# Kernel tuning notes

Hardware: AMD Instinct MI355X
Metric: run time of the kernel (lower is better)

## Reference

```python
import jax, jax.numpy as jnp
import numpy as np

Z_DIM = 1          # coord column zeroed before coalescing (module default)
GRID = 512         # max coordinate value per column (exclusive)


def setup_inputs() -> dict:
    key = jax.random.key(0)
    k1, k2 = jax.random.split(key)
    N, C = 400000, 128
    features = jax.random.normal(k1, (N, C), dtype=jnp.float32)
    coords = jax.random.randint(k2, (N, 4), 0, GRID, dtype=jnp.int32)
    return {"features": features, "coords": coords}


def reference(features, coords):
    # features: [N, C] float, coords: [N, 4] int32
    N = features.shape[0]
    # Zero the z column (BEV flattening), as in flatten_coords[:, z_dim] = 0.
    # Since the z column is identically 0 after zeroing, coalescing the 4-col
    # coords is equivalent to keying on the remaining 3 columns.
    non_z = [i for i in range(4) if i != Z_DIM]
    c0 = coords[:, non_z[0]].astype(jnp.int32)
    c1 = coords[:, non_z[1]].astype(jnp.int32)
    c2 = coords[:, non_z[2]].astype(jnp.int32)
    lin_key = (c0 * GRID + c1) * GRID + c2  # < 512^3 < 2^31, fits int32

    # coalesce(): unique coords + scatter-add of [count | features]
    uniq, inv = jnp.unique(lin_key, size=N, fill_value=-1, return_inverse=True)
    ones = jnp.ones((N, 1), dtype=features.dtype)
    feat_with_cnt = jnp.concatenate([ones, features], axis=1)  # [N, C+1]
    sums = jax.ops.segment_sum(feat_with_cnt, inv.reshape(-1), num_segments=N)  # [N, C+1]

    cnt = sums[:, :1]
    out_features = sums[:, 1:] / jnp.maximum(cnt, 1.0)  # padded rows have cnt=0 -> stay 0

    # Decode unique keys back to 4-column coords (z column = 0).
    d2 = uniq % GRID
    rem = uniq // GRID
    d1 = rem % GRID
    d0 = rem // GRID
    zeros = jnp.zeros_like(d0)
    cols = [None] * 4
    cols[Z_DIM] = zeros
    cols[non_z[0]] = d0
    cols[non_z[1]] = d1
    cols[non_z[2]] = d2
    out_coords = jnp.stack(cols, axis=1).astype(jnp.int32)  # [N, 4], padded rows negative

    return out_features, out_coords, cnt[:, 0]
```

## Files before the change

### kernel.cpp

```cpp
#include <hip/hip_runtime.h>


#define NWORDS      (1u << 22)
#define SCAN_BLOCKS 1024
#define WPB         (NWORDS / SCAN_BLOCKS)
#define WPT         (WPB / 256)

typedef float f32x4 __attribute__((ext_vector_type(4)));
typedef unsigned u32;

__global__ void k_build(const int4* __restrict__ coords, u32* __restrict__ bitmap,
                        u32* __restrict__ keys, float* __restrict__ cnt,
                        u32* __restrict__ ctrs, int N) {
    int i = blockIdx.x * blockDim.x + threadIdx.x;
    if (i == 0) { ctrs[0] = 0u; ctrs[1] = 0u; }
    if (i >= N) return;
    int4 c = coords[i];
    u32 key = ((u32)c.x << 18) | ((u32)c.z << 9) | (u32)c.w;
    keys[i] = key;
    cnt[i] = 0.0f;
    atomicOr(&bitmap[key >> 5], 1u << (key & 31u));
}

__global__ void k_scan1(const u32* __restrict__ bitmap, u32* __restrict__ blockSums) {
    __shared__ u32 sd[256];
    const uint4* bm = (const uint4*)(bitmap + (size_t)blockIdx.x * WPB + (size_t)threadIdx.x * WPT);
    u32 s = 0;
#pragma unroll
    for (int k = 0; k < WPT / 4; ++k) {
        uint4 v = bm[k];
        s += __popc(v.x) + __popc(v.y) + __popc(v.z) + __popc(v.w);
    }
    sd[threadIdx.x] = s;
    __syncthreads();
    for (int off = 128; off > 0; off >>= 1) {
        if ((int)threadIdx.x < off) sd[threadIdx.x] += sd[threadIdx.x + off];
        __syncthreads();
    }
    if (threadIdx.x == 0) blockSums[blockIdx.x] = sd[0];
}

__global__ void k_scan2(const u32* __restrict__ blockSums,
                        u32* __restrict__ blockOffsets,
                        u32* __restrict__ totalM) {
    __shared__ u32 sd[SCAN_BLOCKS];
    int t = threadIdx.x;
    u32 v = blockSums[t];
    sd[t] = v;
    __syncthreads();
    for (int off = 1; off < SCAN_BLOCKS; off <<= 1) {
        u32 add = (t >= off) ? sd[t - off] : 0u;
        __syncthreads();
        sd[t] += add;
        __syncthreads();
    }
    blockOffsets[t] = sd[t] - v;
    if (t == SCAN_BLOCKS - 1) totalM[0] = sd[t];
}

__global__ void k_scan3enum(const u32* __restrict__ bitmap,
                            const u32* __restrict__ blockOffsets,
                            uint2* __restrict__ pairs,
                            float4* __restrict__ outc) {
    __shared__ u32 sd[256];
    size_t base = (size_t)blockIdx.x * WPB + (size_t)threadIdx.x * WPT;
    const uint4* bm = (const uint4*)(bitmap + base);
    u32 w[WPT];
    u32 s = 0;
#pragma unroll
    for (int k = 0; k < WPT / 4; ++k) {
        uint4 v = bm[k];
        w[k * 4 + 0] = v.x; w[k * 4 + 1] = v.y; w[k * 4 + 2] = v.z; w[k * 4 + 3] = v.w;
        s += __popc(v.x) + __popc(v.y) + __popc(v.z) + __popc(v.w);
    }
    int t = threadIdx.x;
    sd[t] = s;
    __syncthreads();
    for (int off = 1; off < 256; off <<= 1) {
        u32 add = (t >= off) ? sd[t - off] : 0u;
        __syncthreads();
        sd[t] += add;
        __syncthreads();
    }
    u32 run = blockOffsets[blockIdx.x] + sd[t] - s;
#pragma unroll
    for (int k = 0; k < WPT; ++k) {
        u32 bits = w[k];
        pairs[base + k] = make_uint2(run, bits);
        while (bits) {
            int b = __ffs(bits) - 1;
            u32 key = ((u32)(base + k) << 5) | (u32)b;
            outc[run] = make_float4((float)(key >> 18), 0.f,
                                    (float)((key >> 9) & 511u), (float)(key & 511u));
            ++run;
            bits &= bits - 1u;
        }
    }
}

__global__ void __launch_bounds__(256) k_scatter(
        const f32x4* __restrict__ fin, const u32* __restrict__ keys,
        const uint2* __restrict__ pairs, float* __restrict__ cnt,
        u32* __restrict__ srcElem, uint2* __restrict__ dupElem,
        u32* __restrict__ dupSeg, u32* __restrict__ ctrs,
        f32x4* __restrict__ fout, int N) {
    int gid = blockIdx.x * blockDim.x + threadIdx.x;
    int elem = gid >> 5;
    if (elem >= N) return;
    int c4 = gid & 31;
    u32 s = 0;
    if ((threadIdx.x & 31) == 0) {
        u32 key = keys[elem];
        uint2 p = pairs[key >> 5];
        s = p.x + __popc(p.y & ((1u << (key & 31u)) - 1u));
        float old = atomicAdd(&cnt[s], 1.0f);
        if (old == 0.0f) {
            srcElem[s] = (u32)elem;
        } else {
            u32 di = atomicAdd(&ctrs[0], 1u);
            dupElem[di] = make_uint2((u32)elem, s);
            if (old == 1.0f) {
                u32 ds = atomicAdd(&ctrs[1], 1u);
                dupSeg[ds] = s;
            }
        }
    }
    s = (u32)__shfl((int)s, threadIdx.x & 32);
    f32x4 v = __builtin_nontemporal_load(&fin[(size_t)elem * 32 + c4]);
    fout[(size_t)s * 32 + c4] = v;
}

__global__ void k_fix1(const u32* __restrict__ dupSeg, const u32* __restrict__ ctrs,
                       const u32* __restrict__ totalM,
                       f32x4* __restrict__ fout, float4* __restrict__ outc, int N) {
    u32 nds = ctrs[1];
    u32 M = totalM[0];
    u32 npad = (u32)N - M;
    u32 total = nds + npad;
    int gid = blockIdx.x * blockDim.x + threadIdx.x;
    int c4 = gid & 31;
    u32 stride = (gridDim.x * blockDim.x) >> 5;
    f32x4 z = {0.f, 0.f, 0.f, 0.f};
    for (u32 r = (u32)(gid >> 5); r < total; r += stride) {
        bool pad = (r >= nds);
        u32 row = pad ? (M + r - nds) : dupSeg[r];
        fout[(size_t)row * 32 + c4] = z;
        if (pad && c4 == 0) outc[row] = make_float4(-1.f, 0.f, 511.f, 511.f);
    }
}

__global__ void k_fix2(const f32x4* __restrict__ fin, const uint2* __restrict__ dupElem,
                       const u32* __restrict__ dupSeg, const u32* __restrict__ srcElem,
                       const float* __restrict__ cnt, const u32* __restrict__ ctrs,
                       f32x4* __restrict__ fout) {
    u32 nde = ctrs[0], nds = ctrs[1];
    u32 total = nde + nds;
    int gid = blockIdx.x * blockDim.x + threadIdx.x;
    int c4 = gid & 31;
    u32 stride = (gridDim.x * blockDim.x) >> 5;
    for (u32 t = (u32)(gid >> 5); t < total; t += stride) {
        u32 e, s;
        if (t < nde) { uint2 d = dupElem[t]; e = d.x; s = d.y; }
        else         { s = dupSeg[t - nde]; e = srcElem[s]; }
        float inv = 1.0f / cnt[s];
        f32x4 v = fin[(size_t)e * 32 + c4];
        float* dst = (float*)&fout[(size_t)s * 32 + c4];
        atomicAdd(dst + 0, v.x * inv);
        atomicAdd(dst + 1, v.y * inv);
        atomicAdd(dst + 2, v.z * inv);
        atomicAdd(dst + 3, v.w * inv);
    }
}

extern "C" void kernel_launch(void* const* d_in, const int* in_sizes, int n_in,
                              void* d_out, int out_size, void* d_ws, size_t ws_size,
                              hipStream_t stream) {
    const f32x4* feat_in = (const f32x4*)d_in[0];
    const int4* coords = (const int4*)d_in[1];
    int N = in_sizes[1] / 4;

    float* out = (float*)d_out;
    f32x4* out_feat = (f32x4*)out;
    float4* out_coords = (float4*)(out + (size_t)N * 128);
    float* out_cnt = out + (size_t)N * 132;

    u32* bitmap = (u32*)d_ws;
    uint2* pairs = (uint2*)(bitmap + NWORDS);
    u32* keys = (u32*)(pairs + NWORDS);
    u32* srcElem = keys + N;
    u32* dupSeg = srcElem + N;
    uint2* dupElem = (uint2*)(dupSeg + 65536);
    u32* blockSums = (u32*)(dupElem + 65536);
    u32* blockOffsets = blockSums + SCAN_BLOCKS;
    u32* totalM = blockOffsets + SCAN_BLOCKS;
    u32* ctrs = totalM + 1;

    int nb = (N + 255) / 256;

    hipMemsetAsync(bitmap, 0, (size_t)NWORDS * 4, stream);

    k_build<<<nb, 256, 0, stream>>>(coords, bitmap, keys, out_cnt, ctrs, N);
    k_scan1<<<SCAN_BLOCKS, 256, 0, stream>>>(bitmap, blockSums);
    k_scan2<<<1, SCAN_BLOCKS, 0, stream>>>(blockSums, blockOffsets, totalM);
    k_scan3enum<<<SCAN_BLOCKS, 256, 0, stream>>>(bitmap, blockOffsets, pairs, out_coords);
    k_scatter<<<(int)(((size_t)N * 32 + 255) / 256), 256, 0, stream>>>(
        feat_in, keys, pairs, out_cnt, srcElem, dupElem, dupSeg, ctrs, out_feat, N);
    k_fix1<<<256, 256, 0, stream>>>(dupSeg, ctrs, totalM, out_feat, out_coords, N);
    k_fix2<<<256, 256, 0, stream>>>(feat_in, dupElem, dupSeg, srcElem, out_cnt, ctrs, out_feat);
}
```

Measured before the change: 159.9 us.

## Fuse block counting into build, merge scan kernels, replace atomic fixup with search

The build kernel now counts newly set bits per scan block with atomics, so the separate popcount pass over the bitmap goes away. The block-level prefix is recomputed inside each enumeration block, which removes the single-block scan kernel. The two fixup kernels are merged into one, and each duplicated segment is summed by linearly searching the whole duplicate-element list instead of using float atomics. This cuts three launches and one full bitmap read, but adds a serial loop per duplicate segment that grows with the number of duplicates.

New measurement: 271.9 us. 70.1% more time.

```diff
diff --git a/kernel.cpp b/kernel.cpp
--- a/kernel.cpp
+++ b/kernel.cpp
@@ -11,7 +11,7 @@
 
 __global__ void k_build(const int4* __restrict__ coords, u32* __restrict__ bitmap,
                         u32* __restrict__ keys, float* __restrict__ cnt,
-                        u32* __restrict__ ctrs, int N) {
+                        u32* __restrict__ blockSums, u32* __restrict__ ctrs, int N) {
     int i = blockIdx.x * blockDim.x + threadIdx.x;
     if (i == 0) { ctrs[0] = 0u; ctrs[1] = 0u; }
     if (i >= N) return;
@@ -19,51 +19,42 @@
     u32 key = ((u32)c.x << 18) | ((u32)c.z << 9) | (u32)c.w;
     keys[i] = key;
     cnt[i] = 0.0f;
-    atomicOr(&bitmap[key >> 5], 1u << (key & 31u));
+    u32 bit = 1u << (key & 31u);
+    u32 old = atomicOr(&bitmap[key >> 5], bit);
+    if (!(old & bit)) atomicAdd(&blockSums[key >> 17], 1u);
 }
 
-__global__ void k_scan1(const u32* __restrict__ bitmap, u32* __restrict__ blockSums) {
+__global__ void k_scanenum(const u32* __restrict__ bitmap,
+                           const u32* __restrict__ blockSums,
+                           uint2* __restrict__ pairs,
+                           float4* __restrict__ outc,
+                           u32* __restrict__ totalM) {
     __shared__ u32 sd[256];
-    const uint4* bm = (const uint4*)(bitmap + (size_t)blockIdx.x * WPB + (size_t)threadIdx.x * WPT);
-    u32 s = 0;
-#pragma unroll
-    for (int k = 0; k < WPT / 4; ++k) {
-        uint4 v = bm[k];
-        s += __popc(v.x) + __popc(v.y) + __popc(v.z) + __popc(v.w);
-    }
-    sd[threadIdx.x] = s;
+    __shared__ u32 pfx[SCAN_BLOCKS];
+    const int t = threadIdx.x;
+    const int bid = blockIdx.x;
+
+    uint4 bs = ((const uint4*)blockSums)[t];
+    u32 ls = bs.x + bs.y + bs.z + bs.w;
+    sd[t] = ls;
     __syncthreads();
-    for (int off = 128; off > 0; off >>= 1) {
-        if ((int)threadIdx.x < off) sd[threadIdx.x] += sd[threadIdx.x + off];
-        __syncthreads();
-    }
-    if (threadIdx.x == 0) blockSums[blockIdx.x] = sd[0];
-}
-
-__global__ void k_scan2(const u32* __restrict__ blockSums,
-                        u32* __restrict__ blockOffsets,
-                        u32* __restrict__ totalM) {
-    __shared__ u32 sd[SCAN_BLOCKS];
-    int t = threadIdx.x;
-    u32 v = blockSums[t];
-    sd[t] = v;
-    __syncthreads();
-    for (int off = 1; off < SCAN_BLOCKS; off <<= 1) {
+    for (int off = 1; off < 256; off <<= 1) {
         u32 add = (t >= off) ? sd[t - off] : 0u;
         __syncthreads();
         sd[t] += add;
         __syncthreads();
     }
-    blockOffsets[t] = sd[t] - v;
-    if (t == SCAN_BLOCKS - 1) totalM[0] = sd[t];
-}
+    u32 ex = sd[t] - ls;
+    pfx[t * 4 + 0] = ex;
+    pfx[t * 4 + 1] = ex + bs.x;
+    pfx[t * 4 + 2] = ex + bs.x + bs.y;
+    pfx[t * 4 + 3] = ex + bs.x + bs.y + bs.z;
+    if (bid == 0 && t == 255) totalM[0] = sd[255];
+    __syncthreads();
+    const u32 blockBase = pfx[bid];
+    __syncthreads();
 
-__global__ void k_scan3enum(const u32* __restrict__ bitmap,
-                            const u32* __restrict__ blockOffsets,
-                            uint2* __restrict__ pairs,
-                            float4* __restrict__ outc) {
-    __shared__ u32 sd[256];
-    size_t base = (size_t)blockIdx.x * WPB + (size_t)threadIdx.x * WPT;
+    size_t base = (size_t)bid * WPB + (size_t)t * WPT;
     const uint4* bm = (const uint4*)(bitmap + base);
     u32 w[WPT];
     u32 s = 0;
@@ -73,7 +64,6 @@
         w[k * 4 + 0] = v.x; w[k * 4 + 1] = v.y; w[k * 4 + 2] = v.z; w[k * 4 + 3] = v.w;
         s += __popc(v.x) + __popc(v.y) + __popc(v.z) + __popc(v.w);
     }
-    int t = threadIdx.x;
     sd[t] = s;
     __syncthreads();
     for (int off = 1; off < 256; off <<= 1) {
@@ -82,7 +72,7 @@
         sd[t] += add;
         __syncthreads();
     }
-    u32 run = blockOffsets[blockIdx.x] + sd[t] - s;
+    u32 run = blockBase + sd[t] - s;
 #pragma unroll
     for (int k = 0; k < WPT; ++k) {
         u32 bits = w[k];
@@ -130,45 +120,35 @@
     fout[(size_t)s * 32 + c4] = v;
 }
 
-__global__ void k_fix1(const u32* __restrict__ dupSeg, const u32* __restrict__ ctrs,
-                       const u32* __restrict__ totalM,
-                       f32x4* __restrict__ fout, float4* __restrict__ outc, int N) {
-    u32 nds = ctrs[1];
+__global__ void k_fix(const f32x4* __restrict__ fin, const uint2* __restrict__ dupElem,
+                      const u32* __restrict__ dupSeg, const u32* __restrict__ srcElem,
+                      const float* __restrict__ cnt, const u32* __restrict__ ctrs,
+                      const u32* __restrict__ totalM,
+                      f32x4* __restrict__ fout, float4* __restrict__ outc, int N) {
+    u32 nde = ctrs[0], nds = ctrs[1];
     u32 M = totalM[0];
     u32 npad = (u32)N - M;
     u32 total = nds + npad;
     int gid = blockIdx.x * blockDim.x + threadIdx.x;
     int c4 = gid & 31;
     u32 stride = (gridDim.x * blockDim.x) >> 5;
-    f32x4 z = {0.f, 0.f, 0.f, 0.f};
     for (u32 r = (u32)(gid >> 5); r < total; r += stride) {
-        bool pad = (r >= nds);
-        u32 row = pad ? (M + r - nds) : dupSeg[r];
-        fout[(size_t)row * 32 + c4] = z;
-        if (pad && c4 == 0) outc[row] = make_float4(-1.f, 0.f, 511.f, 511.f);
-    }
-}
-
-__global__ void k_fix2(const f32x4* __restrict__ fin, const uint2* __restrict__ dupElem,
-                       const u32* __restrict__ dupSeg, const u32* __restrict__ srcElem,
-                       const float* __restrict__ cnt, const u32* __restrict__ ctrs,
-                       f32x4* __restrict__ fout) {
-    u32 nde = ctrs[0], nds = ctrs[1];
-    u32 total = nde + nds;
-    int gid = blockIdx.x * blockDim.x + threadIdx.x;
-    int c4 = gid & 31;
-    u32 stride = (gridDim.x * blockDim.x) >> 5;
-    for (u32 t = (u32)(gid >> 5); t < total; t += stride) {
-        u32 e, s;
-        if (t < nde) { uint2 d = dupElem[t]; e = d.x; s = d.y; }
-        else         { s = dupSeg[t - nde]; e = srcElem[s]; }
-        float inv = 1.0f / cnt[s];
-        f32x4 v = fin[(size_t)e * 32 + c4];
-        float* dst = (float*)&fout[(size_t)s * 32 + c4];
-        atomicAdd(dst + 0, v.x * inv);
-        atomicAdd(dst + 1, v.y * inv);
-        atomicAdd(dst + 2, v.z * inv);
-        atomicAdd(dst + 3, v.w * inv);
+        if (r < nds) {
+            u32 s = dupSeg[r];
+            f32x4 acc = fin[(size_t)srcElem[s] * 32 + c4];
+            for (u32 k = 0; k < nde; ++k) {
+                uint2 d = dupElem[k];
+                if (d.y == s) acc += fin[(size_t)d.x * 32 + c4];
+            }
+            float inv = 1.0f / cnt[s];
+            acc *= inv;
+            fout[(size_t)s * 32 + c4] = acc;
+        } else {
+            u32 row = M + (r - nds);
+            f32x4 z = {0.f, 0.f, 0.f, 0.f};
+            fout[(size_t)row * 32 + c4] = z;
+            if (c4 == 0) outc[row] = make_float4(-1.f, 0.f, 511.f, 511.f);
+        }
     }
 }
 
@@ -185,26 +165,23 @@
     float* out_cnt = out + (size_t)N * 132;
 
     u32* bitmap = (u32*)d_ws;
-    uint2* pairs = (uint2*)(bitmap + NWORDS);
+    u32* blockSums = bitmap + NWORDS;
+    uint2* pairs = (uint2*)(blockSums + SCAN_BLOCKS);
     u32* keys = (u32*)(pairs + NWORDS);
     u32* srcElem = keys + N;
     u32* dupSeg = srcElem + N;
     uint2* dupElem = (uint2*)(dupSeg + 65536);
-    u32* blockSums = (u32*)(dupElem + 65536);
-    u32* blockOffsets = blockSums + SCAN_BLOCKS;
-    u32* totalM = blockOffsets + SCAN_BLOCKS;
+    u32* totalM = (u32*)(dupElem + 65536);
     u32* ctrs = totalM + 1;
 
     int nb = (N + 255) / 256;
 
-    hipMemsetAsync(bitmap, 0, (size_t)NWORDS * 4, stream);
+    hipMemsetAsync(bitmap, 0, (size_t)NWORDS * 4 + SCAN_BLOCKS * 4, stream);
 
-    k_build<<<nb, 256, 0, stream>>>(coords, bitmap, keys, out_cnt, ctrs, N);
-    k_scan1<<<SCAN_BLOCKS, 256, 0, stream>>>(bitmap, blockSums);
-    k_scan2<<<1, SCAN_BLOCKS, 0, stream>>>(blockSums, blockOffsets, totalM);
-    k_scan3enum<<<SCAN_BLOCKS, 256, 0, stream>>>(bitmap, blockOffsets, pairs, out_coords);
+    k_build<<<nb, 256, 0, stream>>>(coords, bitmap, keys, out_cnt, blockSums, ctrs, N);
+    k_scanenum<<<SCAN_BLOCKS, 256, 0, stream>>>(bitmap, blockSums, pairs, out_coords, totalM);
     k_scatter<<<(int)(((size_t)N * 32 + 255) / 256), 256, 0, stream>>>(
         feat_in, keys, pairs, out_cnt, srcElem, dupElem, dupSeg, ctrs, out_feat, N);
-    k_fix1<<<256, 256, 0, stream>>>(dupSeg, ctrs, totalM, out_feat, out_coords, N);
-    k_fix2<<<256, 256, 0, stream>>>(feat_in, dupElem, dupSeg, srcElem, out_cnt, ctrs, out_feat);
+    k_fix<<<256, 256, 0, stream>>>(feat_in, dupElem, dupSeg, srcElem, out_cnt, ctrs,
+                                   totalM, out_feat, out_coords, N);
 }
```
